# Optimization experiments

Measured on AMD Instinct MI355X. Metric: run time of the kernel, lower is better.

Reference implementation:

```python
import jax, jax.numpy as jnp
import numpy as np

N = 50000        # n_nodes
E = 1_600_000    # n_edges (avg degree 32)
IN = 128         # in_dim
H = 8            # num_heads
R = 16           # hidden_rank
D = 16           # out_dim (per head)
SCALE = float(np.sqrt(D))


def setup_inputs() -> dict:
    key = jax.random.key(0)
    k1, k2, k3, k4, k5, k6 = jax.random.split(key, 6)
    h = jax.random.normal(k1, (N, IN), jnp.float32)
    src = jax.random.randint(k2, (E,), 0, N, dtype=jnp.int32)
    dst = jax.random.randint(k3, (E,), 0, N, dtype=jnp.int32)
    s = 1.0 / np.sqrt(IN)  # kaiming-ish scale
    p = jax.random.normal(k4, (IN, H * R), jnp.float32) * s
    q = jax.random.normal(k5, (IN, H * R), jnp.float32) * s
    Wv = jax.random.normal(k6, (IN, H * D), jnp.float32) * s
    return {"h": h, "src": src, "dst": dst, "p": p, "q": q, "Wv": Wv}


def reference(h, src, dst, p, q, Wv):
    # global_attention_type == 'transform' -> atted = h
    K = (h @ q).reshape(N, H, R)   # K_h = atted @ _q
    Q = (h @ p).reshape(N, H, R)   # Q_h = h @ _p
    V = (h @ Wv).reshape(N, H, D)  # V_h = V(h), no bias
    # per-edge score: (K[src] * Q[dst]).sum(-1, keepdim), then scaled exp
    score = jnp.sum(K[src] * Q[dst], axis=-1, keepdims=True)   # [E, H, 1]
    score = jnp.exp(jnp.clip(score / SCALE, -5.0, 5.0))
    # scatter-sum into destination nodes
    wV = jax.ops.segment_sum(V[src] * score, dst, num_segments=N)  # [N, H, D]
    z = jax.ops.segment_sum(score, dst, num_segments=N)            # [N, H, 1]
    z = jnp.where(z == 0, jnp.float32(0.001), z)
    return wV / z
```

## Files before the change

### kernel.cpp

```cpp
#include <hip/hip_runtime.h>
#include <hip/hip_fp16.h>


#define HNODE 64
#define EPB   4096
#define BKT_SHIFT 7
#define BKT_CAP 5120

typedef _Float16 f16x8 __attribute__((ext_vector_type(8)));
typedef float    f32x4 __attribute__((ext_vector_type(4)));
typedef _Float16 hv2   __attribute__((ext_vector_type(2)));

__device__ __forceinline__ float fdot2(unsigned a, unsigned b, float c) {
#if __has_builtin(__builtin_amdgcn_fdot2)
    return __builtin_amdgcn_fdot2(__builtin_bit_cast(hv2, a),
                                  __builtin_bit_cast(hv2, b), c, false);
#else
    __half2 ah = *(__half2*)&a, bh = *(__half2*)&b;
    float2 af = __half22float2(ah), bf = __half22float2(bh);
    return c + af.x * bf.x + af.y * bf.y;
#endif
}

__device__ __forceinline__ float2 h2f(unsigned u) {
    __half2 hh = *(__half2*)&u;
    return __half22float2(hh);
}

__device__ __forceinline__ unsigned pack2(float a, float b) {
    __half2 hh = __floats2half2_rn(a, b);
    return *(unsigned*)&hh;
}

__device__ __forceinline__ float clamp5(float x) {
#if __has_builtin(__builtin_amdgcn_fmed3f)
    return __builtin_amdgcn_fmed3f(x, -5.f, 5.f);
#else
    return fminf(fmaxf(x, -5.f), 5.f);
#endif
}

#if __has_builtin(__builtin_amdgcn_mov_dpp)
#define QBCAST(v, J) __builtin_amdgcn_mov_dpp((v), (J) * 0x55, 0xF, 0xF, true)
__device__ __forceinline__ float qadd_xor1(float x) {
    int y = __builtin_amdgcn_mov_dpp(__float_as_int(x), 0xB1, 0xF, 0xF, true);
    return x + __int_as_float(y);
}
__device__ __forceinline__ float qadd_xor2(float x) {
    int y = __builtin_amdgcn_mov_dpp(__float_as_int(x), 0x4E, 0xF, 0xF, true);
    return x + __int_as_float(y);
}
#else
#define QBCAST(v, J) __shfl((v), ((threadIdx.x & 63) & ~3) + (J), 64)
__device__ __forceinline__ float qadd_xor1(float x) { return x + __shfl_xor(x, 1); }
__device__ __forceinline__ float qadd_xor2(float x) { return x + __shfl_xor(x, 2); }
#endif

__global__ __launch_bounds__(256) void wt_convert_kernel(
    const float* __restrict__ Wq, const float* __restrict__ Wp,
    const float* __restrict__ Wv, __half* __restrict__ Wt,
    int* __restrict__ btot, int nbkt)
{
    int o = blockIdx.x * 256 + threadIdx.x;
    if (o < 49152) {
        int m = o >> 14, rem = o & 16383;
        int nn = rem >> 7, kk = rem & 127;
        const float* W = (m == 0) ? Wq : (m == 1) ? Wp : Wv;
        Wt[o] = __float2half(W[kk * 128 + nn]);
    } else {
        int i = o - 49152;
        if (i < nbkt) btot[i] = 0;
    }
}

__global__ __launch_bounds__(256) void gemm_scatter_kernel(
    const float* __restrict__ h, const __half* __restrict__ Wt,
    unsigned* __restrict__ KV, __half* __restrict__ Q, int n,
    const int* __restrict__ src, const int* __restrict__ dst,
    unsigned* __restrict__ gcsr, int* __restrict__ btot,
    int E, int nbkt, int gemm_blocks)
{
    __shared__ __align__(16) char smem[34816];
    const int t = threadIdx.x;

    if ((int)blockIdx.x < gemm_blocks) {
        _Float16* ws = (_Float16*)smem;
        const int wid = t >> 6, lane = t & 63;
        const int node0 = blockIdx.x * HNODE;
        const int mrow = lane & 15, quad = lane >> 4;

        const int row = node0 + wid * 16 + mrow;
        const bool rowvalid = (row < n);
        const int rowc = rowvalid ? row : (n - 1);

        f16x8 hfr[4];
        #pragma unroll
        for (int s = 0; s < 4; s++) {
            const float4* hp = (const float4*)(h + (size_t)rowc * 128 + quad * 8 + 32 * s);
            float4 f0 = hp[0], f1 = hp[1];
            f16x8 a;
            a[0] = (_Float16)f0.x; a[1] = (_Float16)f0.y;
            a[2] = (_Float16)f0.z; a[3] = (_Float16)f0.w;
            a[4] = (_Float16)f1.x; a[5] = (_Float16)f1.y;
            a[6] = (_Float16)f1.z; a[7] = (_Float16)f1.w;
            hfr[s] = a;
        }

        f32x4 acc[3][8];
        #pragma unroll
        for (int m = 0; m < 3; m++)
            #pragma unroll
            for (int ct = 0; ct < 8; ct++) acc[m][ct] = (f32x4){0.f, 0.f, 0.f, 0.f};

        #pragma unroll
        for (int m = 0; m < 3; m++) {
            __syncthreads();
            {
                const uint4* wg = (const uint4*)(Wt + (size_t)m * 16384);
                #pragma unroll
                for (int i = 0; i < 8; i++) {
                    int idx = t * 8 + i;
                    int r = idx >> 4, seg = idx & 15;
                    *(uint4*)(ws + r * 136 + seg * 8) = wg[idx];
                }
            }
            __syncthreads();
            #pragma unroll
            for (int s = 0; s < 4; s++) {
                #pragma unroll
                for (int ct = 0; ct < 8; ct++) {
                    f16x8 a = *(const f16x8*)(ws + (ct * 16 + mrow) * 136 + quad * 8 + 32 * s);
                    acc[m][ct] = __builtin_amdgcn_mfma_f32_16x16x32_f16(a, hfr[s], acc[m][ct], 0, 0, 0);
                }
            }
        }

        if (rowvalid) {
            #pragma unroll
            for (int ct = 0; ct < 8; ct++) {
                uint4 ov;
                ov.x = pack2(acc[0][ct][0], acc[0][ct][1]);
                ov.y = pack2(acc[0][ct][2], acc[0][ct][3]);
                ov.z = pack2(acc[2][ct][0], acc[2][ct][1]);
                ov.w = pack2(acc[2][ct][2], acc[2][ct][3]);
                *(uint4*)(KV + (((size_t)ct * n + row) << 4) + 4 * quad) = ov;
                uint2 qv;
                qv.x = pack2(acc[1][ct][0], acc[1][ct][1]);
                qv.y = pack2(acc[1][ct][2], acc[1][ct][3]);
                *(uint2*)(Q + (((size_t)ct * n + row) << 4) + 4 * quad) = qv;
            }
        }
    } else {
        int* cnt     = (int*)smem;
        int* base_sh = (int*)(smem + 2048);

        int blk = blockIdx.x - gemm_blocks;
        for (int i = t; i < 512; i += 256) cnt[i] = 0;
        __syncthreads();

        int4 sv[4], dv[4], rk[4];
        int base = blk * EPB + t * 4;
        #pragma unroll
        for (int r = 0; r < 4; r++) {
            int i = base + r * 1024;
            if (i + 3 < E) {
                sv[r] = *(const int4*)(src + i);
                dv[r] = *(const int4*)(dst + i);
            } else {
                int tsrc[4], tdst[4];
                for (int k = 0; k < 4; k++) {
                    int j = i + k;
                    tsrc[k] = (j < E) ? src[j] : 0;
                    tdst[k] = (j < E) ? dst[j] : -1;
                }
                sv[r] = make_int4(tsrc[0], tsrc[1], tsrc[2], tsrc[3]);
                dv[r] = make_int4(tdst[0], tdst[1], tdst[2], tdst[3]);
            }
            rk[r].x = (dv[r].x >= 0) ? atomicAdd(&cnt[dv[r].x >> BKT_SHIFT], 1) : 0;
            rk[r].y = (dv[r].y >= 0) ? atomicAdd(&cnt[dv[r].y >> BKT_SHIFT], 1) : 0;
            rk[r].z = (dv[r].z >= 0) ? atomicAdd(&cnt[dv[r].z >> BKT_SHIFT], 1) : 0;
            rk[r].w = (dv[r].w >= 0) ? atomicAdd(&cnt[dv[r].w >> BKT_SHIFT], 1) : 0;
        }
        __syncthreads();

        for (int i = t; i < nbkt; i += 256) {
            int c = cnt[i];
            base_sh[i] = (c > 0) ? atomicAdd(&btot[i], c) : 0;
        }
        __syncthreads();

        #pragma unroll
        for (int r = 0; r < 4; r++) {
            int s, d, bb, pos;
            d = dv[r].x; if (d >= 0) { s = sv[r].x; bb = d >> BKT_SHIFT; pos = base_sh[bb] + rk[r].x; if (pos < BKT_CAP) gcsr[(size_t)bb * BKT_CAP + pos] = ((unsigned)(d & 127) << 18) | (unsigned)s; }
            d = dv[r].y; if (d >= 0) { s = sv[r].y; bb = d >> BKT_SHIFT; pos = base_sh[bb] + rk[r].y; if (pos < BKT_CAP) gcsr[(size_t)bb * BKT_CAP + pos] = ((unsigned)(d & 127) << 18) | (unsigned)s; }
            d = dv[r].z; if (d >= 0) { s = sv[r].z; bb = d >> BKT_SHIFT; pos = base_sh[bb] + rk[r].z; if (pos < BKT_CAP) gcsr[(size_t)bb * BKT_CAP + pos] = ((unsigned)(d & 127) << 18) | (unsigned)s; }
            d = dv[r].w; if (d >= 0) { s = sv[r].w; bb = d >> BKT_SHIFT; pos = base_sh[bb] + rk[r].w; if (pos < BKT_CAP) gcsr[(size_t)bb * BKT_CAP + pos] = ((unsigned)(d & 127) << 18) | (unsigned)s; }
        }
    }
}

__global__ __launch_bounds__(512) void fine2_kernel(
    const unsigned* __restrict__ gcsr, const int* __restrict__ btot,
    int2* __restrict__ offs, unsigned short* __restrict__ csr,
    int* __restrict__ nodeord, int N)
{
    __shared__ unsigned sedge[BKT_CAP];
    __shared__ unsigned short srank[BKT_CAP];
    __shared__ unsigned short lcsr[BKT_CAP];
    __shared__ int ldeg[128];
    __shared__ int lstart[128];
    __shared__ int ts[128];

    const int b = blockIdx.x, t = threadIdx.x;
    const int seg0 = b * BKT_CAP;

    int tot = btot[b];
    if (tot > BKT_CAP) tot = BKT_CAP;

    if (t < 128) ldeg[t] = 0;
    __syncthreads();

    const unsigned* gb = gcsr + (size_t)b * BKT_CAP;
    for (int i = t; i < tot; i += 512) {
        unsigned w = gb[i];
        sedge[i] = w;
        srank[i] = (unsigned short)atomicAdd(&ldeg[w >> 18], 1);
    }
    __syncthreads();

    int mydeg = (t < 128) ? ldeg[t] : 0;
    if (t < 128) ts[t] = mydeg;
    __syncthreads();
    for (int off = 1; off < 128; off <<= 1) {
        int x = (t < 128) ? ts[t] : 0;
        int y = (t >= off && t < 128) ? ts[t - off] : 0;
        __syncthreads();
        if (t < 128) ts[t] = x + y;
        __syncthreads();
    }
    if (t < 128) {
        int lbeg = ts[t] - mydeg;
        lstart[t] = lbeg;
        int node = (b << 7) + t;
        if (node < N) offs[node] = make_int2(seg0 + lbeg, seg0 + lbeg + mydeg);
        int r = 0;
        for (int j = 0; j < 128; j++) {
            int dj = ldeg[j];
            r += (int)((dj > mydeg) || (dj == mydeg && j < t));
        }
        nodeord[(b << 7) + r] = t;
    }
    __syncthreads();

    for (int i = t; i < tot; i += 512) {
        unsigned w = sedge[i];
        lcsr[lstart[w >> 18] + srank[i]] = (unsigned short)(w & 0xFFFFu);
    }
    __syncthreads();

    for (int i = t; i < tot; i += 512)
        csr[seg0 + i] = lcsr[i];
}

#define AGG_COMPUTE(A, J)                                                      \
    {                                                                          \
        float s = fdot2(A.x, qq.x, fdot2(A.y, qq.y, 0.f));                     \
        s = qadd_xor1(s);                                                      \
        s = qadd_xor2(s);                                                      \
        float xx = clamp5(s * 0.25f);                                          \
        float sc = (e + (J) < cnt) ? __expf(xx) : 0.f;                         \
        accz += sc;                                                            \
        float2 v0 = h2f(A.z), v1 = h2f(A.w);                                   \
        av0 += sc * v0.x; av1 += sc * v0.y;                                    \
        av2 += sc * v1.x; av3 += sc * v1.y;                                    \
    }

__global__ __launch_bounds__(256) void aggregate_kernel(
    const unsigned* __restrict__ KVh,
    const uint2* __restrict__ Qr,
    const int2* __restrict__ offs, const unsigned short* __restrict__ csr,
    const int* __restrict__ nodeord,
    float* __restrict__ out, int n)
{
    const int t = threadIdx.x;
    const int head = blockIdx.x & 7;
    const int rest = blockIdx.x >> 3;
    const int bkt = rest >> 1, sub = rest & 1;
    const int lane = t & 63;
    const int g = lane >> 2;
    const int p = lane & 3;
    const int chunk = ((t >> 6) << 1) | sub;

    const int spos = (bkt << 7) + (chunk << 4) + g;
    const int local = nodeord[spos];
    const int node = (bkt << 7) + local;
    const bool nvalid = (node < n);
    const int nodec = nvalid ? node : 0;

    int beg = 0, cnt = 0;
    if (nvalid) {
        int2 be = offs[node];
        beg = be.x; cnt = be.y - be.x;
    }

    const size_t hn = (size_t)head * n;
    const uint2 qq = Qr[(hn + nodec) * 4 + p];
    const char* kvb = (const char*)KVh + hn * 64;
    const unsigned ppo = (unsigned)p << 4;

    float accz = 0.f;
    float av0 = 0.f, av1 = 0.f, av2 = 0.f, av3 = 0.f;

    const int cl = (cnt > 0) ? (cnt - 1) : 0;

    int np = (p < cl) ? p : cl;
    int idxA = (int)csr[beg + np];
    uint4 a0, a1, a2, a3;
    {
        unsigned j;
        j = (unsigned)QBCAST(idxA, 0); a0 = *(const uint4*)(kvb + ((j << 6) | ppo));
        j = (unsigned)QBCAST(idxA, 1); a1 = *(const uint4*)(kvb + ((j << 6) | ppo));
        j = (unsigned)QBCAST(idxA, 2); a2 = *(const uint4*)(kvb + ((j << 6) | ppo));
        j = (unsigned)QBCAST(idxA, 3); a3 = *(const uint4*)(kvb + ((j << 6) | ppo));
    }
    np = 4 + p; np = (np < cl) ? np : cl;
    int idxB = (int)csr[beg + np];

    for (int e = 0; e < cnt; e += 4) {
        unsigned j;
        uint4 b0, b1, b2, b3;
        j = (unsigned)QBCAST(idxB, 0); b0 = *(const uint4*)(kvb + ((j << 6) | ppo));
        j = (unsigned)QBCAST(idxB, 1); b1 = *(const uint4*)(kvb + ((j << 6) | ppo));
        j = (unsigned)QBCAST(idxB, 2); b2 = *(const uint4*)(kvb + ((j << 6) | ppo));
        j = (unsigned)QBCAST(idxB, 3); b3 = *(const uint4*)(kvb + ((j << 6) | ppo));
        np = e + 8 + p; np = (np < cl) ? np : cl;
        idxB = (int)csr[beg + np];

        AGG_COMPUTE(a0, 0)
        AGG_COMPUTE(a1, 1)
        AGG_COMPUTE(a2, 2)
        AGG_COMPUTE(a3, 3)

        a0 = b0; a1 = b1; a2 = b2; a3 = b3;
    }

    if (nvalid) {
        float z = accz;
        if (z == 0.f) z = 0.001f;
        float inv = 1.0f / z;
        *(float4*)(out + (size_t)node * 128 + head * 16 + p * 4) =
            make_float4(av0 * inv, av1 * inv, av2 * inv, av3 * inv);
    }
}


extern "C" void kernel_launch(void* const* d_in, const int* in_sizes, int n_in,
                              void* d_out, int out_size, void* d_ws, size_t ws_size,
                              hipStream_t stream)
{
    const float* h   = (const float*)d_in[0];
    const int*   src = (const int*)d_in[1];
    const int*   dst = (const int*)d_in[2];
    const float* p   = (const float*)d_in[3];
    const float* q   = (const float*)d_in[4];
    const float* wv  = (const float*)d_in[5];
    float* out = (float*)d_out;

    const int N = in_sizes[0] / 128;
    const int E = in_sizes[1];
    const int nbkt = (N + 127) >> BKT_SHIFT;
    const int nblk_e = (E + EPB - 1) / EPB;
    const int gemm_blocks = (N + HNODE - 1) / HNODE;

    unsigned* KV = (unsigned*)d_ws;
    __half* Qh   = (__half*)(KV + (size_t)N * 128);
    unsigned* gcsr = (unsigned*)(Qh + (size_t)N * 128);
    int* btot    = (int*)(gcsr + (size_t)nbkt * BKT_CAP);
    unsigned short* csr16 = (unsigned short*)(btot + 512);
    int2* offs   = (int2*)(csr16 + (size_t)nbkt * BKT_CAP);
    int* nodeord = (int*)(offs + N);
    __half* Wt   = (__half*)(nodeord + (size_t)nbkt * 128);

    wt_convert_kernel<<<194, 256, 0, stream>>>(q, p, wv, Wt, btot, nbkt);

    gemm_scatter_kernel<<<gemm_blocks + nblk_e, 256, 0, stream>>>(
        h, Wt, KV, Qh, N, src, dst, gcsr, btot, E, nbkt, gemm_blocks);

    fine2_kernel<<<nbkt, 512, 0, stream>>>(gcsr, btot, offs, csr16, nodeord, N);

    aggregate_kernel<<<nbkt * 16, 256, 0, stream>>>(
        KV, (const uint2*)Qh, offs, csr16, nodeord, (float*)out, N);
}
```

Baseline: 216.3 us.

## Enlarge scatter blocks to 16K edges with ranks staged in shared memory

Each scatter block now handles four times as many edges, so there are fewer blocks doing global atomics on bucket totals and the bucket runs each block writes are longer and more contiguous. Per-edge ranks move from registers into a shared-memory ushort buffer, and src/dst are read again in the second pass instead of being held in registers. The cost is less block-level parallelism in the scatter phase, a second global read of dst, and a larger shared allocation, which may reduce occupancy for the GEMM blocks that share this kernel.

New measurement: 232.9 us. 1.08x slower.

```diff
diff --git a/kernel.cpp b/kernel.cpp
--- a/kernel.cpp
+++ b/kernel.cpp
@@ -3,7 +3,7 @@
 
 
 #define HNODE 64
-#define EPB   4096
+#define EPB   16384
 #define BKT_SHIFT 7
 #define BKT_CAP 5120
 
@@ -80,7 +80,7 @@
     unsigned* __restrict__ gcsr, int* __restrict__ btot,
     int E, int nbkt, int gemm_blocks)
 {
-    __shared__ __align__(16) char smem[34816];
+    __shared__ __align__(16) char smem[36864];
     const int t = threadIdx.x;
 
     if ((int)blockIdx.x < gemm_blocks) {
@@ -153,33 +153,30 @@
     } else {
         int* cnt     = (int*)smem;
         int* base_sh = (int*)(smem + 2048);
+        unsigned short* rkbuf = (unsigned short*)(smem + 4096);
 
         int blk = blockIdx.x - gemm_blocks;
         for (int i = t; i < 512; i += 256) cnt[i] = 0;
         __syncthreads();
 
-        int4 sv[4], dv[4], rk[4];
-        int base = blk * EPB + t * 4;
-        #pragma unroll
-        for (int r = 0; r < 4; r++) {
-            int i = base + r * 1024;
+        const int base = blk * EPB;
+
+        for (int r = 0; r < 16; r++) {
+            int li = r * 1024 + t * 4;
+            int i = base + li;
+            int4 dv;
             if (i + 3 < E) {
-                sv[r] = *(const int4*)(src + i);
-                dv[r] = *(const int4*)(dst + i);
+                dv = *(const int4*)(dst + i);
             } else {
-                int tsrc[4], tdst[4];
-                for (int k = 0; k < 4; k++) {
-                    int j = i + k;
-                    tsrc[k] = (j < E) ? src[j] : 0;
-                    tdst[k] = (j < E) ? dst[j] : -1;
-                }
-                sv[r] = make_int4(tsrc[0], tsrc[1], tsrc[2], tsrc[3]);
-                dv[r] = make_int4(tdst[0], tdst[1], tdst[2], tdst[3]);
+                dv.x = (i     < E) ? dst[i]     : -1;
+                dv.y = (i + 1 < E) ? dst[i + 1] : -1;
+                dv.z = (i + 2 < E) ? dst[i + 2] : -1;
+                dv.w = (i + 3 < E) ? dst[i + 3] : -1;
             }
-            rk[r].x = (dv[r].x >= 0) ? atomicAdd(&cnt[dv[r].x >> BKT_SHIFT], 1) : 0;
-            rk[r].y = (dv[r].y >= 0) ? atomicAdd(&cnt[dv[r].y >> BKT_SHIFT], 1) : 0;
-            rk[r].z = (dv[r].z >= 0) ? atomicAdd(&cnt[dv[r].z >> BKT_SHIFT], 1) : 0;
-            rk[r].w = (dv[r].w >= 0) ? atomicAdd(&cnt[dv[r].w >> BKT_SHIFT], 1) : 0;
+            rkbuf[li + 0] = (dv.x >= 0) ? (unsigned short)atomicAdd(&cnt[dv.x >> BKT_SHIFT], 1) : 0;
+            rkbuf[li + 1] = (dv.y >= 0) ? (unsigned short)atomicAdd(&cnt[dv.y >> BKT_SHIFT], 1) : 0;
+            rkbuf[li + 2] = (dv.z >= 0) ? (unsigned short)atomicAdd(&cnt[dv.z >> BKT_SHIFT], 1) : 0;
+            rkbuf[li + 3] = (dv.w >= 0) ? (unsigned short)atomicAdd(&cnt[dv.w >> BKT_SHIFT], 1) : 0;
         }
         __syncthreads();
 
@@ -189,13 +186,28 @@
         }
         __syncthreads();
 
-        #pragma unroll
-        for (int r = 0; r < 4; r++) {
+        for (int r = 0; r < 16; r++) {
+            int li = r * 1024 + t * 4;
+            int i = base + li;
+            int4 sv, dv;
+            if (i + 3 < E) {
+                sv = *(const int4*)(src + i);
+                dv = *(const int4*)(dst + i);
+            } else {
+                sv.x = (i     < E) ? src[i]     : 0;
+                sv.y = (i + 1 < E) ? src[i + 1] : 0;
+                sv.z = (i + 2 < E) ? src[i + 2] : 0;
+                sv.w = (i + 3 < E) ? src[i + 3] : 0;
+                dv.x = (i     < E) ? dst[i]     : -1;
+                dv.y = (i + 1 < E) ? dst[i + 1] : -1;
+                dv.z = (i + 2 < E) ? dst[i + 2] : -1;
+                dv.w = (i + 3 < E) ? dst[i + 3] : -1;
+            }
             int s, d, bb, pos;
-            d = dv[r].x; if (d >= 0) { s = sv[r].x; bb = d >> BKT_SHIFT; pos = base_sh[bb] + rk[r].x; if (pos < BKT_CAP) gcsr[(size_t)bb * BKT_CAP + pos] = ((unsigned)(d & 127) << 18) | (unsigned)s; }
-            d = dv[r].y; if (d >= 0) { s = sv[r].y; bb = d >> BKT_SHIFT; pos = base_sh[bb] + rk[r].y; if (pos < BKT_CAP) gcsr[(size_t)bb * BKT_CAP + pos] = ((unsigned)(d & 127) << 18) | (unsigned)s; }
-            d = dv[r].z; if (d >= 0) { s = sv[r].z; bb = d >> BKT_SHIFT; pos = base_sh[bb] + rk[r].z; if (pos < BKT_CAP) gcsr[(size_t)bb * BKT_CAP + pos] = ((unsigned)(d & 127) << 18) | (unsigned)s; }
-            d = dv[r].w; if (d >= 0) { s = sv[r].w; bb = d >> BKT_SHIFT; pos = base_sh[bb] + rk[r].w; if (pos < BKT_CAP) gcsr[(size_t)bb * BKT_CAP + pos] = ((unsigned)(d & 127) << 18) | (unsigned)s; }
+            d = dv.x; if (d >= 0) { s = sv.x; bb = d >> BKT_SHIFT; pos = base_sh[bb] + rkbuf[li + 0]; if (pos < BKT_CAP) gcsr[(size_t)bb * BKT_CAP + pos] = ((unsigned)(d & 127) << 18) | (unsigned)s; }
+            d = dv.y; if (d >= 0) { s = sv.y; bb = d >> BKT_SHIFT; pos = base_sh[bb] + rkbuf[li + 1]; if (pos < BKT_CAP) gcsr[(size_t)bb * BKT_CAP + pos] = ((unsigned)(d & 127) << 18) | (unsigned)s; }
+            d = dv.z; if (d >= 0) { s = sv.z; bb = d >> BKT_SHIFT; pos = base_sh[bb] + rkbuf[li + 2]; if (pos < BKT_CAP) gcsr[(size_t)bb * BKT_CAP + pos] = ((unsigned)(d & 127) << 18) | (unsigned)s; }
+            d = dv.w; if (d >= 0) { s = sv.w; bb = d >> BKT_SHIFT; pos = base_sh[bb] + rkbuf[li + 3]; if (pos < BKT_CAP) gcsr[(size_t)bb * BKT_CAP + pos] = ((unsigned)(d & 127) << 18) | (unsigned)s; }
         }
     }
 }
```

## Regroup kernels: scatter with weight conversion, GEMM with bucket sort

Applied to the files above, without the earlier changes.

Moves the edge bucket scatter into the weight-conversion kernel and moves the projection GEMM into the fine per-bucket CSR build kernel, so independent work shares a launch. The bucket-counter zeroing becomes a memset. The GEMM now runs with 512 threads and 128 nodes per block, which changes its occupancy and shared-memory use. The intent is to overlap the latency-bound sort stages with the GEMM and cut one dependency step, at the cost of an extra memset launch and mixed block types in one kernel.

After: 211.9 us. 2.0% less time.

```diff
diff --git a/kernel.cpp b/kernel.cpp
--- a/kernel.cpp
+++ b/kernel.cpp
@@ -2,7 +2,6 @@
 #include <hip/hip_fp16.h>
 
 
-#define HNODE 64
 #define EPB   4096
 #define BKT_SHIFT 7
 #define BKT_CAP 5120
@@ -56,105 +55,25 @@
 __device__ __forceinline__ float qadd_xor2(float x) { return x + __shfl_xor(x, 2); }
 #endif
 
-__global__ __launch_bounds__(256) void wt_convert_kernel(
+__global__ __launch_bounds__(256) void prep_kernel(
     const float* __restrict__ Wq, const float* __restrict__ Wp,
     const float* __restrict__ Wv, __half* __restrict__ Wt,
-    int* __restrict__ btot, int nbkt)
+    const int* __restrict__ src, const int* __restrict__ dst,
+    unsigned* __restrict__ gcsr, int* __restrict__ btot,
+    int E, int nbkt)
 {
-    int o = blockIdx.x * 256 + threadIdx.x;
-    if (o < 49152) {
+    __shared__ int cnt[512];
+    __shared__ int base_sh[512];
+    const int t = threadIdx.x;
+
+    if ((int)blockIdx.x < 192) {
+        int o = blockIdx.x * 256 + t;
         int m = o >> 14, rem = o & 16383;
         int nn = rem >> 7, kk = rem & 127;
         const float* W = (m == 0) ? Wq : (m == 1) ? Wp : Wv;
         Wt[o] = __float2half(W[kk * 128 + nn]);
     } else {
-        int i = o - 49152;
-        if (i < nbkt) btot[i] = 0;
-    }
-}
-
-__global__ __launch_bounds__(256) void gemm_scatter_kernel(
-    const float* __restrict__ h, const __half* __restrict__ Wt,
-    unsigned* __restrict__ KV, __half* __restrict__ Q, int n,
-    const int* __restrict__ src, const int* __restrict__ dst,
-    unsigned* __restrict__ gcsr, int* __restrict__ btot,
-    int E, int nbkt, int gemm_blocks)
-{
-    __shared__ __align__(16) char smem[34816];
-    const int t = threadIdx.x;
-
-    if ((int)blockIdx.x < gemm_blocks) {
-        _Float16* ws = (_Float16*)smem;
-        const int wid = t >> 6, lane = t & 63;
-        const int node0 = blockIdx.x * HNODE;
-        const int mrow = lane & 15, quad = lane >> 4;
-
-        const int row = node0 + wid * 16 + mrow;
-        const bool rowvalid = (row < n);
-        const int rowc = rowvalid ? row : (n - 1);
-
-        f16x8 hfr[4];
-        #pragma unroll
-        for (int s = 0; s < 4; s++) {
-            const float4* hp = (const float4*)(h + (size_t)rowc * 128 + quad * 8 + 32 * s);
-            float4 f0 = hp[0], f1 = hp[1];
-            f16x8 a;
-            a[0] = (_Float16)f0.x; a[1] = (_Float16)f0.y;
-            a[2] = (_Float16)f0.z; a[3] = (_Float16)f0.w;
-            a[4] = (_Float16)f1.x; a[5] = (_Float16)f1.y;
-            a[6] = (_Float16)f1.z; a[7] = (_Float16)f1.w;
-            hfr[s] = a;
-        }
-
-        f32x4 acc[3][8];
-        #pragma unroll
-        for (int m = 0; m < 3; m++)
-            #pragma unroll
-            for (int ct = 0; ct < 8; ct++) acc[m][ct] = (f32x4){0.f, 0.f, 0.f, 0.f};
-
-        #pragma unroll
-        for (int m = 0; m < 3; m++) {
-            __syncthreads();
-            {
-                const uint4* wg = (const uint4*)(Wt + (size_t)m * 16384);
-                #pragma unroll
-                for (int i = 0; i < 8; i++) {
-                    int idx = t * 8 + i;
-                    int r = idx >> 4, seg = idx & 15;
-                    *(uint4*)(ws + r * 136 + seg * 8) = wg[idx];
-                }
-            }
-            __syncthreads();
-            #pragma unroll
-            for (int s = 0; s < 4; s++) {
-                #pragma unroll
-                for (int ct = 0; ct < 8; ct++) {
-                    f16x8 a = *(const f16x8*)(ws + (ct * 16 + mrow) * 136 + quad * 8 + 32 * s);
-                    acc[m][ct] = __builtin_amdgcn_mfma_f32_16x16x32_f16(a, hfr[s], acc[m][ct], 0, 0, 0);
-                }
-            }
-        }
-
-        if (rowvalid) {
-            #pragma unroll
-            for (int ct = 0; ct < 8; ct++) {
-                uint4 ov;
-                ov.x = pack2(acc[0][ct][0], acc[0][ct][1]);
-                ov.y = pack2(acc[0][ct][2], acc[0][ct][3]);
-                ov.z = pack2(acc[2][ct][0], acc[2][ct][1]);
-                ov.w = pack2(acc[2][ct][2], acc[2][ct][3]);
-                *(uint4*)(KV + (((size_t)ct * n + row) << 4) + 4 * quad) = ov;
-                uint2 qv;
-                qv.x = pack2(acc[1][ct][0], acc[1][ct][1]);
-                qv.y = pack2(acc[1][ct][2], acc[1][ct][3]);
-                *(uint2*)(Q + (((size_t)ct * n + row) << 4) + 4 * quad) = qv;
-            }
-        }
-    } else {
-        int* cnt     = (int*)smem;
-        int* base_sh = (int*)(smem + 2048);
-
-        int blk = blockIdx.x - gemm_blocks;
+        int blk = blockIdx.x - 192;
         for (int i = t; i < 512; i += 256) cnt[i] = 0;
         __syncthreads();
 
@@ -200,67 +119,141 @@
     }
 }
 
-__global__ __launch_bounds__(512) void fine2_kernel(
+__global__ __launch_bounds__(512) void gemm_fine2_kernel(
+    const float* __restrict__ h, const __half* __restrict__ Wt,
+    unsigned* __restrict__ KV, __half* __restrict__ Q, int n,
     const unsigned* __restrict__ gcsr, const int* __restrict__ btot,
     int2* __restrict__ offs, unsigned short* __restrict__ csr,
-    int* __restrict__ nodeord, int N)
+    int* __restrict__ nodeord, int nbkt)
 {
-    __shared__ unsigned sedge[BKT_CAP];
-    __shared__ unsigned short srank[BKT_CAP];
-    __shared__ unsigned short lcsr[BKT_CAP];
-    __shared__ int ldeg[128];
-    __shared__ int lstart[128];
-    __shared__ int ts[128];
-
-    const int b = blockIdx.x, t = threadIdx.x;
-    const int seg0 = b * BKT_CAP;
-
-    int tot = btot[b];
-    if (tot > BKT_CAP) tot = BKT_CAP;
-
-    if (t < 128) ldeg[t] = 0;
-    __syncthreads();
-
-    const unsigned* gb = gcsr + (size_t)b * BKT_CAP;
-    for (int i = t; i < tot; i += 512) {
-        unsigned w = gb[i];
-        sedge[i] = w;
-        srank[i] = (unsigned short)atomicAdd(&ldeg[w >> 18], 1);
-    }
-    __syncthreads();
-
-    int mydeg = (t < 128) ? ldeg[t] : 0;
-    if (t < 128) ts[t] = mydeg;
-    __syncthreads();
-    for (int off = 1; off < 128; off <<= 1) {
-        int x = (t < 128) ? ts[t] : 0;
-        int y = (t >= off && t < 128) ? ts[t - off] : 0;
-        __syncthreads();
-        if (t < 128) ts[t] = x + y;
-        __syncthreads();
-    }
-    if (t < 128) {
-        int lbeg = ts[t] - mydeg;
-        lstart[t] = lbeg;
-        int node = (b << 7) + t;
-        if (node < N) offs[node] = make_int2(seg0 + lbeg, seg0 + lbeg + mydeg);
-        int r = 0;
-        for (int j = 0; j < 128; j++) {
-            int dj = ldeg[j];
-            r += (int)((dj > mydeg) || (dj == mydeg && j < t));
-        }
-        nodeord[(b << 7) + r] = t;
-    }
-    __syncthreads();
-
-    for (int i = t; i < tot; i += 512) {
-        unsigned w = sedge[i];
-        lcsr[lstart[w >> 18] + srank[i]] = (unsigned short)(w & 0xFFFFu);
-    }
-    __syncthreads();
-
-    for (int i = t; i < tot; i += 512)
-        csr[seg0 + i] = lcsr[i];
+    __shared__ __align__(16) char smem[42496];
+    const int t = threadIdx.x;
+
+    if ((int)blockIdx.x < nbkt) {
+        unsigned* sedge = (unsigned*)smem;
+        unsigned short* srank = (unsigned short*)(smem + 20480);
+        unsigned short* lcsr  = (unsigned short*)(smem + 30720);
+        int* ldeg   = (int*)(smem + 40960);
+        int* lstart = (int*)(smem + 41472);
+        int* ts     = (int*)(smem + 41984);
+
+        const int b = blockIdx.x;
+        const int seg0 = b * BKT_CAP;
+
+        int tot = btot[b];
+        if (tot > BKT_CAP) tot = BKT_CAP;
+
+        if (t < 128) ldeg[t] = 0;
+        __syncthreads();
+
+        const unsigned* gb = gcsr + (size_t)b * BKT_CAP;
+        for (int i = t; i < tot; i += 512) {
+            unsigned w = gb[i];
+            sedge[i] = w;
+            srank[i] = (unsigned short)atomicAdd(&ldeg[w >> 18], 1);
+        }
+        __syncthreads();
+
+        int mydeg = (t < 128) ? ldeg[t] : 0;
+        if (t < 128) ts[t] = mydeg;
+        __syncthreads();
+        for (int off = 1; off < 128; off <<= 1) {
+            int x = (t < 128) ? ts[t] : 0;
+            int y = (t >= off && t < 128) ? ts[t - off] : 0;
+            __syncthreads();
+            if (t < 128) ts[t] = x + y;
+            __syncthreads();
+        }
+        if (t < 128) {
+            int lbeg = ts[t] - mydeg;
+            lstart[t] = lbeg;
+            int node = (b << 7) + t;
+            if (node < n) offs[node] = make_int2(seg0 + lbeg, seg0 + lbeg + mydeg);
+            int r = 0;
+            for (int j = 0; j < 128; j++) {
+                int dj = ldeg[j];
+                r += (int)((dj > mydeg) || (dj == mydeg && j < t));
+            }
+            nodeord[(b << 7) + r] = t;
+        }
+        __syncthreads();
+
+        for (int i = t; i < tot; i += 512) {
+            unsigned w = sedge[i];
+            lcsr[lstart[w >> 18] + srank[i]] = (unsigned short)(w & 0xFFFFu);
+        }
+        __syncthreads();
+
+        for (int i = t; i < tot; i += 512)
+            csr[seg0 + i] = lcsr[i];
+    } else {
+        _Float16* ws = (_Float16*)smem;
+        const int wid = t >> 6, lane = t & 63;
+        const int node0 = ((int)blockIdx.x - nbkt) * 128;
+        const int mrow = lane & 15, quad = lane >> 4;
+
+        const int row = node0 + wid * 16 + mrow;
+        const bool rowvalid = (row < n);
+        const int rowc = rowvalid ? row : (n - 1);
+
+        f16x8 hfr[4];
+        #pragma unroll
+        for (int s = 0; s < 4; s++) {
+            const float4* hp = (const float4*)(h + (size_t)rowc * 128 + quad * 8 + 32 * s);
+            float4 f0 = hp[0], f1 = hp[1];
+            f16x8 a;
+            a[0] = (_Float16)f0.x; a[1] = (_Float16)f0.y;
+            a[2] = (_Float16)f0.z; a[3] = (_Float16)f0.w;
+            a[4] = (_Float16)f1.x; a[5] = (_Float16)f1.y;
+            a[6] = (_Float16)f1.z; a[7] = (_Float16)f1.w;
+            hfr[s] = a;
+        }
+
+        f32x4 acc[3][8];
+        #pragma unroll
+        for (int m = 0; m < 3; m++)
+            #pragma unroll
+            for (int ct = 0; ct < 8; ct++) acc[m][ct] = (f32x4){0.f, 0.f, 0.f, 0.f};
+
+        #pragma unroll
+        for (int m = 0; m < 3; m++) {
+            __syncthreads();
+            {
+                const uint4* wg = (const uint4*)(Wt + (size_t)m * 16384);
+                #pragma unroll
+                for (int i = 0; i < 4; i++) {
+                    int idx = t * 4 + i;
+                    int r = idx >> 4, seg = idx & 15;
+                    *(uint4*)(ws + r * 136 + seg * 8) = wg[idx];
+                }
+            }
+            __syncthreads();
+            #pragma unroll
+            for (int s = 0; s < 4; s++) {
+                #pragma unroll
+                for (int ct = 0; ct < 8; ct++) {
+                    f16x8 a = *(const f16x8*)(ws + (ct * 16 + mrow) * 136 + quad * 8 + 32 * s);
+                    acc[m][ct] = __builtin_amdgcn_mfma_f32_16x16x32_f16(a, hfr[s], acc[m][ct], 0, 0, 0);
+                }
+            }
+        }
+
+        if (rowvalid) {
+            #pragma unroll
+            for (int ct = 0; ct < 8; ct++) {
+                uint4 ov;
+                ov.x = pack2(acc[0][ct][0], acc[0][ct][1]);
+                ov.y = pack2(acc[0][ct][2], acc[0][ct][3]);
+                ov.z = pack2(acc[2][ct][0], acc[2][ct][1]);
+                ov.w = pack2(acc[2][ct][2], acc[2][ct][3]);
+                *(uint4*)(KV + (((size_t)ct * n + row) << 4) + 4 * quad) = ov;
+                uint2 qv;
+                qv.x = pack2(acc[1][ct][0], acc[1][ct][1]);
+                qv.y = pack2(acc[1][ct][2], acc[1][ct][3]);
+                *(uint2*)(Q + (((size_t)ct * n + row) << 4) + 4 * quad) = qv;
+            }
+        }
+    }
 }
 
 #define AGG_COMPUTE(A, J)                                                      \
@@ -371,7 +364,7 @@
     const int E = in_sizes[1];
     const int nbkt = (N + 127) >> BKT_SHIFT;
     const int nblk_e = (E + EPB - 1) / EPB;
-    const int gemm_blocks = (N + HNODE - 1) / HNODE;
+    const int gemm_blocks = (N + 127) / 128;
 
     unsigned* KV = (unsigned*)d_ws;
     __half* Qh   = (__half*)(KV + (size_t)N * 128);
@@ -382,12 +375,13 @@
     int* nodeord = (int*)(offs + N);
     __half* Wt   = (__half*)(nodeord + (size_t)nbkt * 128);
 
-    wt_convert_kernel<<<194, 256, 0, stream>>>(q, p, wv, Wt, btot, nbkt);
-
-    gemm_scatter_kernel<<<gemm_blocks + nblk_e, 256, 0, stream>>>(
-        h, Wt, KV, Qh, N, src, dst, gcsr, btot, E, nbkt, gemm_blocks);
-
-    fine2_kernel<<<nbkt, 512, 0, stream>>>(gcsr, btot, offs, csr16, nodeord, N);
+    hipMemsetAsync(btot, 0, 512 * sizeof(int), stream);
+
+    prep_kernel<<<192 + nblk_e, 256, 0, stream>>>(
+        q, p, wv, Wt, src, dst, gcsr, btot, E, nbkt);
+
+    gemm_fine2_kernel<<<nbkt + gemm_blocks, 512, 0, stream>>>(
+        h, Wt, KV, Qh, N, gcsr, btot, offs, csr16, nodeord, nbkt);
 
     aggregate_kernel<<<nbkt * 16, 256, 0, stream>>>(
         KV, (const uint2*)Qh, offs, csr16, nodeord, (float*)out, N);
```
